# Performance work log

Hardware: AMD Instinct MI355X
Metric: run time of the kernel (lower is better)

## Reference

```python
import jax, jax.numpy as jnp
import numpy as np

K = 3
STRIDE = 1
PADDING = 1


def unfold(x, k, stride, padding):
    # torch.nn.functional.unfold: patches ordered (C, kh, kw), positions row-major
    N, C, H, W = x.shape
    xp = jnp.pad(x, ((0, 0), (0, 0), (padding, padding), (padding, padding)))
    H_out = (H - k + 2 * padding) // stride + 1
    W_out = (W - k + 2 * padding) // stride + 1
    patches = jnp.stack(
        [xp[:, :, i:i + stride * H_out:stride, j:j + stride * W_out:stride]
         for i in range(k) for j in range(k)],
        axis=2,
    )  # (N, C, k*k, H_out, W_out)
    return patches.reshape(N, C * k * k, H_out * W_out), H_out, W_out


def setup_inputs() -> dict:
    key = jax.random.key(0)
    k1, k2 = jax.random.split(key)
    x = jax.random.normal(k1, (16, 64, 14, 14), dtype=jnp.float32)
    W = jax.random.normal(k2, (64, 64, 3, 3), dtype=jnp.float32)
    return {"x": x, "W": W}


def reference(x, W):
    F_out = W.shape[0]
    X_col, H_out, W_out = unfold(x, K, STRIDE, PADDING)  # (N, D, P)
    W_col = W.reshape(F_out, -1)                          # (F, D)
    # AdderNet: out[n,f,p] = -sum_d |W[f,d] - X[n,d,p]|
    out = -jnp.sum(jnp.abs(W_col[None, :, :, None] - X_col[:, None, :, :]), axis=2)  # (N, F, P)
    return out.reshape(x.shape[0], F_out, H_out, W_out)
```

## Files before the change

### kernel.cpp

```cpp
#include <hip/hip_runtime.h>


#define N_ 16
#define C_ 64
#define F_ 64
#define P_ 196
#define CSTRIDE 60

__global__ __launch_bounds__(256, 1) void adder2d_kernel(
    const float* __restrict__ x, const float* __restrict__ w,
    float* __restrict__ out)
{
    __shared__ __align__(16) float xs[C_ * CSTRIDE];
    __shared__ float part[4][16][15];

    const int tid = threadIdx.x;
    const int row = blockIdx.x;
    const int n   = blockIdx.y;
    const int fg  = blockIdx.z;

    #pragma unroll
    for (int i = 0; i < 12; ++i) {
        const int idx = tid + 256 * i;
        const int c   = idx / 48;
        const int rem = idx - c * 48;
        const int r   = rem >> 4;
        const int col = rem & 15;
        const int ir  = row + r - 1;
        float v = 0.f;
        if (col >= 1 && col <= 14 && ir >= 0 && ir <= 13)
            v = x[(n * C_ + c) * P_ + ir * 14 + (col - 1)];
        xs[c * CSTRIDE + r * 16 + col] = v;
    }

    const int f_local = tid & 15;
    const int c_sub   = (tid >> 4) & 3;
    const int wv      = tid >> 6;
    const int cb      = wv * 16 + c_sub * 4;

    float Wr[36];
    {
        const float4* wp = (const float4*)(w + (fg * 16 + f_local) * (C_ * 9)
                                             + cb * 9);
        #pragma unroll
        for (int i = 0; i < 9; ++i) {
            float4 t = wp[i];
            Wr[4 * i + 0] = t.x; Wr[4 * i + 1] = t.y;
            Wr[4 * i + 2] = t.z; Wr[4 * i + 3] = t.w;
        }
    }

    float acc[14];
    #pragma unroll
    for (int p = 0; p < 14; ++p) acc[p] = 0.f;

    __syncthreads();

    const float* xb = xs + cb * CSTRIDE;
    #pragma unroll
    for (int cl = 0; cl < 4; ++cl) {
        #pragma unroll
        for (int kh = 0; kh < 3; ++kh) {
            const float4* rp = (const float4*)(xb + cl * CSTRIDE + kh * 16);
            float4 q0 = rp[0], q1 = rp[1], q2 = rp[2], q3 = rp[3];
            float xr[16] = {q0.x, q0.y, q0.z, q0.w,  q1.x, q1.y, q1.z, q1.w,
                            q2.x, q2.y, q2.z, q2.w,  q3.x, q3.y, q3.z, q3.w};
            #pragma unroll
            for (int kw = 0; kw < 3; ++kw) {
                const float wvv = Wr[cl * 9 + kh * 3 + kw];
                #pragma unroll
                for (int p = 0; p < 14; ++p)
                    acc[p] += fabsf(wvv - xr[p + kw]);
            }
        }
    }

    #pragma unroll
    for (int p = 0; p < 14; ++p) {
        acc[p] += __shfl_xor(acc[p], 16);
        acc[p] += __shfl_xor(acc[p], 32);
    }

    if (c_sub == 0 && (tid & 15) == f_local) {
        #pragma unroll
        for (int p = 0; p < 14; ++p)
            part[wv][f_local][p] = acc[p];
    }
    __syncthreads();

    if (tid < 224) {
        const int f  = tid / 14;
        const int px = tid - f * 14;
        float s = part[0][f][px] + part[1][f][px]
                + part[2][f][px] + part[3][f][px];
        out[(n * F_ + fg * 16 + f) * P_ + row * 14 + px] = -s;
    }
}

extern "C" void kernel_launch(void* const* d_in, const int* in_sizes, int n_in,
                              void* d_out, int out_size, void* d_ws, size_t ws_size,
                              hipStream_t stream) {
    const float* x = (const float*)d_in[0];
    const float* w = (const float*)d_in[1];
    float* out = (float*)d_out;
    dim3 grid(14, N_, 4);
    adder2d_kernel<<<grid, 256, 0, stream>>>(x, w, out);
}
```

Baseline: 71.02 us.

## Stage weights in padded shared memory and disable unrolling to cut registers

Weights are no longer loaded per thread into a 36-entry register array. The block now copies its 16 filters' weights cooperatively into a padded shared-memory tile (stride 17) and reads three weights per kernel row inside the loop. The outer loops and the input-staging loop are set to unroll 1, which shrinks code size and register pressure. The channel stride shrinks, and the partial-sum buffer reuses the input tile behind an extra barrier. In exchange, the block adds about 39KB of LDS, a strided global weight copy, more LDS reads in the inner loop, and loop overhead from the rolled loops.

```diff
diff --git a/kernel.cpp b/kernel.cpp
--- a/kernel.cpp
+++ b/kernel.cpp
@@ -5,21 +5,21 @@
 #define C_ 64
 #define F_ 64
 #define P_ 196
-#define CSTRIDE 60
+#define CSTRIDE 52
 
 __global__ __launch_bounds__(256, 1) void adder2d_kernel(
     const float* __restrict__ x, const float* __restrict__ w,
     float* __restrict__ out)
 {
     __shared__ __align__(16) float xs[C_ * CSTRIDE];
-    __shared__ float part[4][16][15];
+    __shared__ float wl[9792];
 
     const int tid = threadIdx.x;
     const int row = blockIdx.x;
     const int n   = blockIdx.y;
     const int fg  = blockIdx.z;
 
-    #pragma unroll
+    #pragma unroll 1
     for (int i = 0; i < 12; ++i) {
         const int idx = tid + 256 * i;
         const int c   = idx / 48;
@@ -33,22 +33,18 @@
         xs[c * CSTRIDE + r * 16 + col] = v;
     }
 
+    #pragma unroll 1
+    for (int i = 0; i < 36; ++i) {
+        const int s   = tid + 256 * i;
+        const int fl  = s / 576;
+        const int rem = s - fl * 576;
+        wl[rem * 17 + fl] = w[(fg * 16 + fl) * 576 + rem];
+    }
+
     const int f_local = tid & 15;
     const int c_sub   = (tid >> 4) & 3;
     const int wv      = tid >> 6;
     const int cb      = wv * 16 + c_sub * 4;
-
-    float Wr[36];
-    {
-        const float4* wp = (const float4*)(w + (fg * 16 + f_local) * (C_ * 9)
-                                             + cb * 9);
-        #pragma unroll
-        for (int i = 0; i < 9; ++i) {
-            float4 t = wp[i];
-            Wr[4 * i + 0] = t.x; Wr[4 * i + 1] = t.y;
-            Wr[4 * i + 2] = t.z; Wr[4 * i + 3] = t.w;
-        }
-    }
 
     float acc[14];
     #pragma unroll
@@ -57,21 +53,21 @@
     __syncthreads();
 
     const float* xb = xs + cb * CSTRIDE;
-    #pragma unroll
+    const float* wb = wl + (cb * 9) * 17 + f_local;
+    #pragma unroll 1
     for (int cl = 0; cl < 4; ++cl) {
-        #pragma unroll
+        #pragma unroll 1
         for (int kh = 0; kh < 3; ++kh) {
             const float4* rp = (const float4*)(xb + cl * CSTRIDE + kh * 16);
             float4 q0 = rp[0], q1 = rp[1], q2 = rp[2], q3 = rp[3];
+            const float* wp = wb + (cl * 9 + kh * 3) * 17;
+            float w0 = wp[0], w1 = wp[17], w2 = wp[34];
             float xr[16] = {q0.x, q0.y, q0.z, q0.w,  q1.x, q1.y, q1.z, q1.w,
                             q2.x, q2.y, q2.z, q2.w,  q3.x, q3.y, q3.z, q3.w};
             #pragma unroll
-            for (int kw = 0; kw < 3; ++kw) {
-                const float wvv = Wr[cl * 9 + kh * 3 + kw];
-                #pragma unroll
-                for (int p = 0; p < 14; ++p)
-                    acc[p] += fabsf(wvv - xr[p + kw]);
-            }
+            for (int p = 0; p < 14; ++p)
+                acc[p] += fabsf(w0 - xr[p]) + fabsf(w1 - xr[p + 1])
+                        + fabsf(w2 - xr[p + 2]);
         }
     }
 
@@ -81,18 +77,20 @@
         acc[p] += __shfl_xor(acc[p], 32);
     }
 
-    if (c_sub == 0 && (tid & 15) == f_local) {
+    __syncthreads();
+    float* part = xs;
+    if (c_sub == 0) {
         #pragma unroll
         for (int p = 0; p < 14; ++p)
-            part[wv][f_local][p] = acc[p];
+            part[(wv * 16 + f_local) * 15 + p] = acc[p];
     }
     __syncthreads();
 
     if (tid < 224) {
         const int f  = tid / 14;
         const int px = tid - f * 14;
-        float s = part[0][f][px] + part[1][f][px]
-                + part[2][f][px] + part[3][f][px];
+        float s = part[(0 * 16 + f) * 15 + px] + part[(1 * 16 + f) * 15 + px]
+                + part[(2 * 16 + f) * 15 + px] + part[(3 * 16 + f) * 15 + px];
         out[(n * F_ + fg * 16 + f) * P_ + row * 14 + px] = -s;
     }
 }
```

Measured after the change: 78.60 us. 1.11x slower.
